# Kernel optimization log

Hardware: AMD Instinct MI355X
Metric: run time of the kernel (lower is better)

## Reference

```python
import jax, jax.numpy as jnp
import numpy as np

N = 10000      # nodes
E = 160000     # edges (before self-loops)
IN = 128       # in_channels
H, D = 8, 64   # heads, hidden_channels (layer 1)
C = 2          # num_classes (layer 2, heads=1, concat=False)
NEG_SLOPE = 0.2  # PyG GATConv default


def setup_inputs() -> dict:
    key = jax.random.key(0)
    ks = jax.random.split(key, 10)
    s = 0.05
    return {
        "x": jax.random.normal(ks[0], (N, IN), jnp.float32),
        "edge_index": jax.random.randint(ks[1], (2, E), 0, N, dtype=jnp.int32),
        "W1": jax.random.normal(ks[2], (H * D, IN), jnp.float32) * s,
        "a_src1": jax.random.normal(ks[3], (H, D), jnp.float32) * s,
        "a_dst1": jax.random.normal(ks[4], (H, D), jnp.float32) * s,
        "b1": jnp.zeros((H * D,), jnp.float32),
        "W2": jax.random.normal(ks[5], (C, H * D), jnp.float32) * s,
        "a_src2": jax.random.normal(ks[6], (1, C), jnp.float32) * s,
        "a_dst2": jax.random.normal(ks[7], (1, C), jnp.float32) * s,
        "b2": jnp.zeros((C,), jnp.float32),
    }


def _gat_conv(x, edge_index, W, a_src, a_dst, bias, concat):
    """PyG-style GATConv (add_self_loops=True, eval mode so no dropout)."""
    n = x.shape[0]
    heads, d = a_src.shape
    h = (x @ W.T).reshape(n, heads, d)          # [N, H, D]
    # add self-loops
    loops = jnp.arange(n, dtype=edge_index.dtype)
    src = jnp.concatenate([edge_index[0], loops])
    dst = jnp.concatenate([edge_index[1], loops])
    # attention logits
    alpha_s = jnp.einsum('nhd,hd->nh', h, a_src)   # [N, H]
    alpha_d = jnp.einsum('nhd,hd->nh', h, a_dst)
    e = jax.nn.leaky_relu(alpha_s[src] + alpha_d[dst], NEG_SLOPE)  # [E+N, H]
    # segment softmax over destination node
    m = jax.lax.stop_gradient(jax.ops.segment_max(e, dst, num_segments=n))
    ex = jnp.exp(e - m[dst])
    denom = jax.ops.segment_sum(ex, dst, num_segments=n)
    alpha = ex / (denom[dst] + 1e-16)               # [E+N, H]
    # weighted scatter-aggregate of source messages
    out = jax.ops.segment_sum(h[src] * alpha[:, :, None], dst, num_segments=n)  # [N,H,D]
    out = out.reshape(n, heads * d) if concat else out.mean(axis=1)
    return out + bias


def reference(x, edge_index, W1, a_src1, a_dst1, b1, W2, a_src2, a_dst2, b2):
    h = jax.nn.elu(_gat_conv(x, edge_index, W1, a_src1, a_dst1, b1, concat=True))
    # dropout p=0.3 is identity in eval mode
    return _gat_conv(h, edge_index, W2, a_src2, a_dst2, b2, concat=False)
```

## Files before the change

kernel.cpp:

```cpp
#include <hip/hip_runtime.h>
#include <float.h>
#include <math.h>

#define NEG 0.2f
#define CAP 64

typedef _Float16 half2_t __attribute__((ext_vector_type(2)));

__device__ inline float bflo(unsigned u) { return __uint_as_float(u << 16); }
__device__ inline float bfhi(unsigned u) { return __uint_as_float(u & 0xffff0000u); }
__device__ inline unsigned packbf2(float a, float b) {
  unsigned ua = __float_as_uint(a), ub = __float_as_uint(b);
  ua = (ua + 0x7fffu + ((ua >> 16) & 1u)) >> 16;
  ub = (ub + 0x7fffu + ((ub >> 16) & 1u)) & 0xffff0000u;
  return ua | ub;
}
__device__ inline unsigned packh2(float a, float b) {
  union { half2_t h; unsigned u; } x;
  x.h = half2_t{(_Float16)a, (_Float16)b};
  return x.u;
}
__device__ inline half2_t u2h(unsigned u) {
  union { unsigned u; half2_t h; } x;
  x.u = u;
  return x.h;
}

__global__ void k_init(int* __restrict__ deg, int* __restrict__ adj, int n) {
  int i = blockIdx.x * 256 + threadIdx.x;
  if (i < n) { deg[i] = 1; adj[i * CAP] = i; }
}

__global__ __launch_bounds__(256) void k_gemm_scatter(
    const float* __restrict__ x, const float* __restrict__ W1,
    const float* __restrict__ a_s, const float* __restrict__ a_d,
    const int* __restrict__ ei, unsigned short* __restrict__ h1b,
    float* __restrict__ as1, float* __restrict__ ad1,
    int* __restrict__ deg, int* __restrict__ adj, int N, int E, int GB) {
  __shared__ unsigned xs[16][36];
  __shared__ unsigned wsl[16][132];
  int bx = blockIdx.x;
  int tid = threadIdx.x;

  if (bx >= GB) {
    int t = (bx - GB) * 256 + tid;
    if (t < E) {
      int s = ei[t], d = ei[E + t];
      int pos = atomicAdd(&deg[d], 1);
      if (pos < CAP) adj[d * CAP + pos] = s;
    }
    return;
  }

  int node0 = (bx >> 2) * 32;
  int cb0 = (bx & 3) * 128;
  int tx = tid & 31, ty = tid >> 5;
  int m0 = ty * 4, n0 = tx * 4;
  const float4* x4 = (const float4*)x;
  const float4* w4 = (const float4*)W1;

  float acc[4][4] = {};
  for (int p = 0; p < 4; p++) {
    __syncthreads();
    {
      int node = tid >> 3, q8 = tid & 7;
      float4 v = make_float4(0.f, 0.f, 0.f, 0.f);
      if (node0 + node < N) v = x4[(size_t)(node0 + node) * 32 + p * 8 + q8];
      xs[q8 * 2 + 0][node] = packh2(v.x, v.y);
      xs[q8 * 2 + 1][node] = packh2(v.z, v.w);
    }
#pragma unroll
    for (int q = 0; q < 4; q++) {
      int idx = tid + q * 256;
      int col = idx >> 3, q8 = idx & 7;
      float4 v = w4[(size_t)(cb0 + col) * 32 + p * 8 + q8];
      wsl[q8 * 2 + 0][col] = packh2(v.x, v.y);
      wsl[q8 * 2 + 1][col] = packh2(v.z, v.w);
    }
    __syncthreads();
#pragma unroll 8
    for (int kp = 0; kp < 16; kp++) {
      uint4 a = *(const uint4*)&xs[kp][m0];
      uint4 b = *(const uint4*)&wsl[kp][n0];
      unsigned av[4] = {a.x, a.y, a.z, a.w};
      unsigned bv[4] = {b.x, b.y, b.z, b.w};
#pragma unroll
      for (int i = 0; i < 4; i++)
#pragma unroll
        for (int j = 0; j < 4; j++)
          acc[i][j] = __builtin_amdgcn_fdot2(u2h(av[i]), u2h(bv[j]), acc[i][j], false);
    }
  }

  int hd = (bx & 3) * 2 + (tx >> 4);
  int c = n0 & 63;
#pragma unroll
  for (int i = 0; i < 4; i++) {
    int node = node0 + m0 + i;
    if (node < N) {
      unsigned w0 = packbf2(acc[i][0], acc[i][1]);
      unsigned w1 = packbf2(acc[i][2], acc[i][3]);
      *(uint2*)&h1b[(size_t)node * 512 + hd * 64 + c] = make_uint2(w0, w1);
    }
  }
  float ps[4], pd[4];
#pragma unroll
  for (int i = 0; i < 4; i++) {
    float s = 0.f, d = 0.f;
#pragma unroll
    for (int j = 0; j < 4; j++) {
      float av = a_s[hd * 64 + c + j];
      float dv = a_d[hd * 64 + c + j];
      s = fmaf(acc[i][j], av, s);
      d = fmaf(acc[i][j], dv, d);
    }
    ps[i] = s; pd[i] = d;
  }
#pragma unroll
  for (int o = 8; o >= 1; o >>= 1) {
#pragma unroll
    for (int i = 0; i < 4; i++) {
      ps[i] += __shfl_xor(ps[i], o);
      pd[i] += __shfl_xor(pd[i], o);
    }
  }
  if ((tx & 15) == 0) {
#pragma unroll
    for (int i = 0; i < 4; i++) {
      int node = node0 + m0 + i;
      if (node < N) { as1[node * 8 + hd] = ps[i]; ad1[node * 8 + hd] = pd[i]; }
    }
  }
}

__global__ __launch_bounds__(256) void k_gat1(
    const uint4* __restrict__ h14, const float* __restrict__ as1,
    const float* __restrict__ ad1, const int* __restrict__ degs,
    const int* __restrict__ adj, const float* __restrict__ b1,
    const float* __restrict__ W2, const float* __restrict__ a_s2,
    const float* __restrict__ a_d2, float2* __restrict__ h2,
    float* __restrict__ as2, float* __restrict__ ad2, int N) {
  int lane = threadIdx.x & 63;
  int n = blockIdx.x * 4 + (threadIdx.x >> 6);
  if (n >= N) return;
  int dg = min(degs[n], CAP);
  const int* arow = adj + n * CAP;
  int j0 = lane >> 3, hh = lane & 7;
  int myh = j0;
  float adv = ad1[n * 8 + hh];

  float den = 0.f;
  float acc[8] = {};
  for (int base = 0; base < dg; base += 8) {
    int j = base + j0;
    float w = 0.f;
    int s = 0;
    if (j < dg) {
      s = arow[j];
      float v = as1[s * 8 + hh] + adv;
      v = v > 0.f ? v : NEG * v;
      w = __expf(v);
      den += w;
    }
    int cnt = min(8, dg - base);
    for (int q = 0; q < cnt; q++) {
      int sq = __shfl(s, q * 8);
      float wq = __shfl(w, q * 8 + myh);
      uint4 qv = h14[(size_t)sq * 64 + lane];
      acc[0] = fmaf(wq, bflo(qv.x), acc[0]);
      acc[1] = fmaf(wq, bfhi(qv.x), acc[1]);
      acc[2] = fmaf(wq, bflo(qv.y), acc[2]);
      acc[3] = fmaf(wq, bfhi(qv.y), acc[3]);
      acc[4] = fmaf(wq, bflo(qv.z), acc[4]);
      acc[5] = fmaf(wq, bfhi(qv.z), acc[5]);
      acc[6] = fmaf(wq, bflo(qv.w), acc[6]);
      acc[7] = fmaf(wq, bfhi(qv.w), acc[7]);
    }
  }
  den += __shfl_xor(den, 8);
  den += __shfl_xor(den, 16);
  den += __shfl_xor(den, 32);
  float dn = __shfl(den, myh) + 1e-16f;
  float inv = 1.0f / dn;

  int c0 = lane * 8;
  float p0 = 0.f, p1 = 0.f;
#pragma unroll
  for (int i = 0; i < 8; i++) {
    float v = fmaf(acc[i], inv, b1[c0 + i]);
    v = v > 0.f ? v : __expf(v) - 1.f;
    p0 = fmaf(v, W2[c0 + i], p0);
    p1 = fmaf(v, W2[512 + c0 + i], p1);
  }
#pragma unroll
  for (int o = 1; o < 64; o <<= 1) {
    p0 += __shfl_xor(p0, o);
    p1 += __shfl_xor(p1, o);
  }
  if (lane == 0) {
    h2[n] = make_float2(p0, p1);
    as2[n] = p0 * a_s2[0] + p1 * a_s2[1];
    ad2[n] = p0 * a_d2[0] + p1 * a_d2[1];
  }
}

__global__ __launch_bounds__(256) void k_gat2(
    const float* __restrict__ h2, const float* __restrict__ as2,
    const float* __restrict__ ad2, const int* __restrict__ degs,
    const int* __restrict__ adj, const float* __restrict__ b2,
    float* __restrict__ out, int N) {
  int lane = threadIdx.x & 63;
  int n = blockIdx.x * 4 + (threadIdx.x >> 6);
  if (n >= N) return;
  int dg = min(degs[n], CAP);
  const int* arow = adj + n * CAP;
  float adn = ad2[n];
  float den = 0.f, n0 = 0.f, n1 = 0.f;
  const float2* h2f = (const float2*)h2;
  for (int j = lane; j < dg; j += 64) {
    int s = arow[j];
    float v = as2[s] + adn;
    v = v > 0.f ? v : NEG * v;
    float w = __expf(v);
    float2 hv = h2f[s];
    den += w;
    n0 = fmaf(w, hv.x, n0);
    n1 = fmaf(w, hv.y, n1);
  }
#pragma unroll
  for (int o = 32; o >= 1; o >>= 1) {
    den += __shfl_xor(den, o);
    n0 += __shfl_xor(n0, o);
    n1 += __shfl_xor(n1, o);
  }
  if (lane == 0) {
    float inv = 1.0f / (den + 1e-16f);
    out[n * 2 + 0] = n0 * inv + b2[0];
    out[n * 2 + 1] = n1 * inv + b2[1];
  }
}

extern "C" void kernel_launch(void* const* d_in, const int* in_sizes, int n_in,
                              void* d_out, int out_size, void* d_ws, size_t ws_size,
                              hipStream_t stream) {
  const float* x    = (const float*)d_in[0];
  const int*   ei   = (const int*)d_in[1];
  const float* W1   = (const float*)d_in[2];
  const float* a_s1 = (const float*)d_in[3];
  const float* a_d1 = (const float*)d_in[4];
  const float* b1   = (const float*)d_in[5];
  const float* W2   = (const float*)d_in[6];
  const float* a_s2 = (const float*)d_in[7];
  const float* a_d2 = (const float*)d_in[8];
  const float* b2   = (const float*)d_in[9];
  int N = in_sizes[0] / 128;
  int E = in_sizes[1] / 2;

  unsigned short* h1b = (unsigned short*)d_ws;
  float*  as1  = (float*)(h1b + (size_t)N * 512);
  float*  ad1  = as1 + (size_t)N * 8;
  float2* h2   = (float2*)(ad1 + (size_t)N * 8);
  float*  as2  = (float*)(h2 + N);
  float*  ad2  = as2 + N;
  int* deg = (int*)(ad2 + N);
  int* adj = deg + N;

  int GB = ((N + 31) / 32) * 4;
  int SB = (E + 255) / 256;

  k_init<<<(N + 255) / 256, 256, 0, stream>>>(deg, adj, N);
  k_gemm_scatter<<<GB + SB, 256, 0, stream>>>(x, W1, a_s1, a_d1, ei, h1b, as1, ad1,
                                              deg, adj, N, E, GB);
  k_gat1<<<(N + 3) / 4, 256, 0, stream>>>((const uint4*)h1b, as1, ad1, deg, adj,
                                          b1, W2, a_s2, a_d2, h2, as2, ad2, N);
  k_gat2<<<(N + 3) / 4, 256, 0, stream>>>((const float*)h2, as2, ad2, deg, adj,
                                          b2, (float*)d_out, N);
}
```

Measured before the change: 68.77 us.

## Use MFMA 16x16x32 f16 for layer-1 projection with 64-node tiles

Replaces the scalar fdot2 GEMM in the fused projection/scatter kernel with MFMA f16 matrix instructions. Each block now stages a full 64-node by 128-column tile with all of K=128 in LDS in one pass, and each wave computes 16 nodes against 128 columns. The aim is to cut ALU cost of the x@W1 projection, at the price of more LDS per block, fewer GEMM blocks, and scattered 2-byte bf16 stores instead of packed vector stores.

Result: faster. 60.43 us (-12.1%).

```diff
diff --git a/kernel.cpp b/kernel.cpp
--- a/kernel.cpp
+++ b/kernel.cpp
@@ -5,25 +5,20 @@
 #define NEG 0.2f
 #define CAP 64
 
+typedef _Float16 f16x8 __attribute__((ext_vector_type(8)));
+typedef float f32x4 __attribute__((ext_vector_type(4)));
 typedef _Float16 half2_t __attribute__((ext_vector_type(2)));
 
 __device__ inline float bflo(unsigned u) { return __uint_as_float(u << 16); }
 __device__ inline float bfhi(unsigned u) { return __uint_as_float(u & 0xffff0000u); }
-__device__ inline unsigned packbf2(float a, float b) {
-  unsigned ua = __float_as_uint(a), ub = __float_as_uint(b);
-  ua = (ua + 0x7fffu + ((ua >> 16) & 1u)) >> 16;
-  ub = (ub + 0x7fffu + ((ub >> 16) & 1u)) & 0xffff0000u;
-  return ua | ub;
+__device__ inline unsigned short bf16of(float f) {
+  unsigned u = __float_as_uint(f);
+  return (unsigned short)((u + 0x7fffu + ((u >> 16) & 1u)) >> 16);
 }
 __device__ inline unsigned packh2(float a, float b) {
   union { half2_t h; unsigned u; } x;
   x.h = half2_t{(_Float16)a, (_Float16)b};
   return x.u;
-}
-__device__ inline half2_t u2h(unsigned u) {
-  union { unsigned u; half2_t h; } x;
-  x.u = u;
-  return x.h;
 }
 
 __global__ void k_init(int* __restrict__ deg, int* __restrict__ adj, int n) {
@@ -37,8 +32,8 @@
     const int* __restrict__ ei, unsigned short* __restrict__ h1b,
     float* __restrict__ as1, float* __restrict__ ad1,
     int* __restrict__ deg, int* __restrict__ adj, int N, int E, int GB) {
-  __shared__ unsigned xs[16][36];
-  __shared__ unsigned wsl[16][132];
+  __shared__ unsigned xs_u[64][68];
+  __shared__ unsigned ws_u[128][68];
   int bx = blockIdx.x;
   int tid = threadIdx.x;
 
@@ -52,83 +47,89 @@
     return;
   }
 
-  int node0 = (bx >> 2) * 32;
-  int cb0 = (bx & 3) * 128;
-  int tx = tid & 31, ty = tid >> 5;
-  int m0 = ty * 4, n0 = tx * 4;
+  int nb = bx >> 2, cb = bx & 3;
+  int node0 = nb * 64;
+  int cb0 = cb * 128;
   const float4* x4 = (const float4*)x;
   const float4* w4 = (const float4*)W1;
 
-  float acc[4][4] = {};
-  for (int p = 0; p < 4; p++) {
-    __syncthreads();
-    {
-      int node = tid >> 3, q8 = tid & 7;
-      float4 v = make_float4(0.f, 0.f, 0.f, 0.f);
-      if (node0 + node < N) v = x4[(size_t)(node0 + node) * 32 + p * 8 + q8];
-      xs[q8 * 2 + 0][node] = packh2(v.x, v.y);
-      xs[q8 * 2 + 1][node] = packh2(v.z, v.w);
-    }
-#pragma unroll
-    for (int q = 0; q < 4; q++) {
-      int idx = tid + q * 256;
-      int col = idx >> 3, q8 = idx & 7;
-      float4 v = w4[(size_t)(cb0 + col) * 32 + p * 8 + q8];
-      wsl[q8 * 2 + 0][col] = packh2(v.x, v.y);
-      wsl[q8 * 2 + 1][col] = packh2(v.z, v.w);
-    }
-    __syncthreads();
-#pragma unroll 8
-    for (int kp = 0; kp < 16; kp++) {
-      uint4 a = *(const uint4*)&xs[kp][m0];
-      uint4 b = *(const uint4*)&wsl[kp][n0];
-      unsigned av[4] = {a.x, a.y, a.z, a.w};
-      unsigned bv[4] = {b.x, b.y, b.z, b.w};
-#pragma unroll
-      for (int i = 0; i < 4; i++)
-#pragma unroll
-        for (int j = 0; j < 4; j++)
-          acc[i][j] = __builtin_amdgcn_fdot2(u2h(av[i]), u2h(bv[j]), acc[i][j], false);
-    }
-  }
-
-  int hd = (bx & 3) * 2 + (tx >> 4);
-  int c = n0 & 63;
-#pragma unroll
-  for (int i = 0; i < 4; i++) {
-    int node = node0 + m0 + i;
-    if (node < N) {
-      unsigned w0 = packbf2(acc[i][0], acc[i][1]);
-      unsigned w1 = packbf2(acc[i][2], acc[i][3]);
-      *(uint2*)&h1b[(size_t)node * 512 + hd * 64 + c] = make_uint2(w0, w1);
-    }
-  }
-  float ps[4], pd[4];
-#pragma unroll
-  for (int i = 0; i < 4; i++) {
-    float s = 0.f, d = 0.f;
-#pragma unroll
-    for (int j = 0; j < 4; j++) {
-      float av = a_s[hd * 64 + c + j];
-      float dv = a_d[hd * 64 + c + j];
-      s = fmaf(acc[i][j], av, s);
-      d = fmaf(acc[i][j], dv, d);
-    }
-    ps[i] = s; pd[i] = d;
+#pragma unroll
+  for (int q = 0; q < 8; q++) {
+    int idx = tid + q * 256;
+    int row = idx >> 5, f4 = idx & 31;
+    float4 v = make_float4(0.f, 0.f, 0.f, 0.f);
+    if (node0 + row < N) v = x4[(size_t)(node0 + row) * 32 + f4];
+    *(uint2*)&xs_u[row][f4 * 2] = make_uint2(packh2(v.x, v.y), packh2(v.z, v.w));
+  }
+#pragma unroll
+  for (int q = 0; q < 16; q++) {
+    int idx = tid + q * 256;
+    int col = idx >> 5, f4 = idx & 31;
+    float4 v = w4[(size_t)(cb0 + col) * 32 + f4];
+    *(uint2*)&ws_u[col][f4 * 2] = make_uint2(packh2(v.x, v.y), packh2(v.z, v.w));
+  }
+  __syncthreads();
+
+  int w = tid >> 6, lane = tid & 63;
+  int r15 = lane & 15, kg = lane >> 4;
+
+  f32x4 acc[8];
+#pragma unroll
+  for (int t = 0; t < 8; t++)
+#pragma unroll
+    for (int e = 0; e < 4; e++) acc[t][e] = 0.f;
+
+  union U { uint4 u; f16x8 h; };
+#pragma unroll
+  for (int ks = 0; ks < 4; ks++) {
+    U a;
+    a.u = *(const uint4*)&xs_u[w * 16 + r15][ks * 16 + kg * 4];
+#pragma unroll
+    for (int t = 0; t < 8; t++) {
+      U b;
+      b.u = *(const uint4*)&ws_u[t * 16 + r15][ks * 16 + kg * 4];
+      acc[t] = __builtin_amdgcn_mfma_f32_16x16x32_f16(a.h, b.h, acc[t], 0, 0, 0);
+    }
+  }
+
+  float psl[4] = {}, pdl[4] = {}, psh[4] = {}, pdh[4] = {};
+#pragma unroll
+  for (int t = 0; t < 8; t++) {
+    int cc = t * 16 + r15;
+    int hd = cb * 2 + (cc >> 6);
+    int c = cc & 63;
+    float asv = a_s[hd * 64 + c];
+    float adv = a_d[hd * 64 + c];
+#pragma unroll
+    for (int i = 0; i < 4; i++) {
+      int node = node0 + w * 16 + kg * 4 + i;
+      float v = acc[t][i];
+      if (node < N) h1b[(size_t)node * 512 + hd * 64 + c] = bf16of(v);
+      if (t < 4) { psl[i] = fmaf(v, asv, psl[i]); pdl[i] = fmaf(v, adv, pdl[i]); }
+      else       { psh[i] = fmaf(v, asv, psh[i]); pdh[i] = fmaf(v, adv, pdh[i]); }
+    }
   }
 #pragma unroll
   for (int o = 8; o >= 1; o >>= 1) {
 #pragma unroll
     for (int i = 0; i < 4; i++) {
-      ps[i] += __shfl_xor(ps[i], o);
-      pd[i] += __shfl_xor(pd[i], o);
-    }
-  }
-  if ((tx & 15) == 0) {
+      psl[i] += __shfl_xor(psl[i], o);
+      pdl[i] += __shfl_xor(pdl[i], o);
+      psh[i] += __shfl_xor(psh[i], o);
+      pdh[i] += __shfl_xor(pdh[i], o);
+    }
+  }
+  if (r15 == 0) {
+    int hd_lo = cb * 2, hd_hi = cb * 2 + 1;
 #pragma unroll
     for (int i = 0; i < 4; i++) {
-      int node = node0 + m0 + i;
-      if (node < N) { as1[node * 8 + hd] = ps[i]; ad1[node * 8 + hd] = pd[i]; }
+      int node = node0 + w * 16 + kg * 4 + i;
+      if (node < N) {
+        as1[node * 8 + hd_lo] = psl[i];
+        ad1[node * 8 + hd_lo] = pdl[i];
+        as1[node * 8 + hd_hi] = psh[i];
+        ad1[node * 8 + hd_hi] = pdh[i];
+      }
     }
   }
 }
@@ -265,7 +266,7 @@
   int* deg = (int*)(ad2 + N);
   int* adj = deg + N;
 
-  int GB = ((N + 31) / 32) * 4;
+  int GB = ((N + 63) / 64) * 4;
   int SB = (E + 255) / 256;
 
   k_init<<<(N + 255) / 256, 256, 0, stream>>>(deg, adj, N);
```
